# Kernel optimization log

Measured on AMD Instinct MI355X. Metric: run time of the kernel, lower is better.

## Reference

```python
import jax, jax.numpy as jnp
import numpy as np

N = 50000      # nodes
E = 60000      # edges
F_IN = 32      # num_features
DIM = 64       # hidden dim
B = 256        # graphs in batch


def setup_inputs() -> dict:
    key = jax.random.key(0)
    ks = jax.random.split(key, 18)
    s = 0.05
    rn = lambda k, shp: (jax.random.normal(k, shp, jnp.float32) * s)
    return {
        "x": jax.random.normal(ks[0], (N, F_IN), jnp.float32),
        "edge_index": jax.random.randint(ks[1], (2, E), 0, N),
        "batch": jnp.sort(jax.random.randint(ks[2], (N,), 0, B)),
        "lin0_w": rn(ks[3], (DIM, F_IN)), "lin0_b": rn(ks[4], (DIM,)),
        "nn1_w": rn(ks[5], (DIM, 1)), "nn1_b": rn(ks[6], (DIM,)),
        "nn2_w": rn(ks[7], (DIM * DIM, DIM)), "nn2_b": rn(ks[8], (DIM * DIM,)),
        "conv_b": rn(ks[9], (DIM,)),
        "gru_w_ih": rn(ks[10], (3 * DIM, DIM)), "gru_w_hh": rn(ks[11], (3 * DIM, DIM)),
        "gru_b_ih": rn(ks[12], (3 * DIM,)), "gru_b_hh": rn(ks[13], (3 * DIM,)),
        "lstm_w_ih": rn(ks[14], (4 * DIM, 2 * DIM)), "lstm_w_hh": rn(ks[15], (4 * DIM, DIM)),
        "lstm_b_ih": rn(ks[16], (4 * DIM,)), "lstm_b_hh": rn(ks[17], (4 * DIM,)),
    }


def reference(x, edge_index, batch, lin0_w, lin0_b, nn1_w, nn1_b, nn2_w, nn2_b,
              conv_b, gru_w_ih, gru_w_hh, gru_b_ih, gru_b_hh,
              lstm_w_ih, lstm_w_hh, lstm_b_ih, lstm_b_hh):
    src, dst = edge_index[0], edge_index[1]
    n_nodes = x.shape[0]
    out = jax.nn.relu(x @ lin0_w.T + lin0_b)          # [N, DIM]
    h = out                                            # GRU hidden state
    edge_attr = jnp.ones((edge_index.shape[1], 1), x.dtype)  # as in source forward
    ones_e = jnp.ones((edge_index.shape[1],), x.dtype)
    deg = jax.ops.segment_sum(ones_e, dst, num_segments=n_nodes)
    inv_deg = jnp.where(deg > 0, 1.0 / jnp.maximum(deg, 1.0), 0.0)[:, None]

    for _ in range(3):
        # edge-conditioned weight: MLP(edge_attr) -> [E, DIM, DIM]
        ew = (jax.nn.relu(edge_attr @ nn1_w.T + nn1_b) @ nn2_w.T + nn2_b)
        ew = ew.reshape(-1, DIM, DIM)
        msg = jnp.einsum('ei,eio->eo', out[src], ew)   # per-edge matvec
        agg = jax.ops.segment_sum(msg, dst, num_segments=n_nodes) * inv_deg  # scatter-mean
        m = jax.nn.relu(agg + conv_b)
        # GRU cell (seq_len = 1)
        gi = m @ gru_w_ih.T + gru_b_ih
        gh = h @ gru_w_hh.T + gru_b_hh
        i_r, i_z, i_n = jnp.split(gi, 3, axis=-1)
        h_r, h_z, h_n = jnp.split(gh, 3, axis=-1)
        r = jax.nn.sigmoid(i_r + h_r)
        z = jax.nn.sigmoid(i_z + h_z)
        n = jnp.tanh(i_n + r * h_n)
        h = (1.0 - z) * n + z * h
        out = h
    feat_map = out

    # Set2Set pooling, 3 processing steps, LSTM(2*DIM -> DIM)
    q_star = jnp.zeros((B, 2 * DIM), x.dtype)
    hl = jnp.zeros((B, DIM), x.dtype)
    cl = jnp.zeros((B, DIM), x.dtype)
    for _ in range(3):
        gates = q_star @ lstm_w_ih.T + lstm_b_ih + hl @ lstm_w_hh.T + lstm_b_hh
        ig, fg, gg, og = jnp.split(gates, 4, axis=-1)  # torch gate order i,f,g,o
        cl = jax.nn.sigmoid(fg) * cl + jax.nn.sigmoid(ig) * jnp.tanh(gg)
        hl = jax.nn.sigmoid(og) * jnp.tanh(cl)
        e = jnp.sum(out * hl[batch], axis=-1)          # [N]
        emax = jax.ops.segment_max(e, batch, num_segments=B)
        emax = jnp.where(jnp.isfinite(emax), emax, 0.0)
        a = jnp.exp(e - emax[batch])
        asum = jax.ops.segment_sum(a, batch, num_segments=B)
        a = a / (asum[batch] + 1e-16)                  # segment softmax
        r_vec = jax.ops.segment_sum(a[:, None] * out, batch, num_segments=B)
        q_star = jnp.concatenate([hl, r_vec], axis=-1)
    return q_star, feat_map
```

## Files before the change

### kernel.cpp

```cpp
#include <hip/hip_runtime.h>
#include <math.h>

#define NN 50000
#define NE 60000
#define FIN 32
#define DIM 64
#define NGB 256
#define SCB 196

typedef short s8v __attribute__((ext_vector_type(8)));
typedef float f4v __attribute__((ext_vector_type(4)));

__device__ __forceinline__ float rl(float v, int lane) {
    return __int_as_float(__builtin_amdgcn_readlane(__float_as_int(v), lane));
}
__device__ __forceinline__ float sigm(float x) { return 1.f / (1.f + expf(-x)); }

__device__ __forceinline__ unsigned int pk2(float a, float b) {
    unsigned int ua = __float_as_uint(a);
    unsigned int ub = __float_as_uint(b);
    ua = (ua + 0x7FFFu + ((ua >> 16) & 1u)) >> 16;
    ub = (ub + 0x7FFFu + ((ub >> 16) & 1u)) & 0xFFFF0000u;
    return ua | ub;
}
__device__ __forceinline__ unsigned short pk1(float a) {
    unsigned int ua = __float_as_uint(a);
    return (unsigned short)((ua + 0x7FFFu + ((ua >> 16) & 1u)) >> 16);
}
__device__ __forceinline__ s8v as_s8(uint4 u) {
    union { uint4 a; s8v b; } c; c.a = u; return c.b;
}

__global__ void k_precompute_W(const float* __restrict__ nn1_w, const float* __restrict__ nn1_b,
                               const float* __restrict__ nn2_w, const float* __restrict__ nn2_b,
                               float* __restrict__ W) {
    __shared__ float t[64];
    int tid = threadIdx.x;
    if (tid < 64) t[tid] = fmaxf(nn1_w[tid] + nn1_b[tid], 0.f);
    __syncthreads();
    int k = blockIdx.x * blockDim.x + tid;
    float acc = nn2_b[k];
    #pragma unroll
    for (int j = 0; j < 64; ++j) acc += t[j] * nn2_w[k * 64 + j];
    W[k] = acc;
}

__global__ void k_pack_mfma(const float* __restrict__ W, const float* __restrict__ wih,
                            const float* __restrict__ whh, const float* __restrict__ bih,
                            const float* __restrict__ bhh, unsigned int* __restrict__ P,
                            float* __restrict__ brz) {
    int q = blockIdx.x * 256 + threadIdx.x;
    if (q < 128) brz[q] = bih[q] + bhh[q];
    if (q < 2048) {
        int byte = q * 4, col = byte >> 7, rem = byte & 127;
        int lin = rem ^ ((col & 7) << 4);
        int k0 = (lin >> 4) * 8 + ((lin >> 2) & 3) * 2;
        P[q] = pk2(W[k0 * 64 + col], W[(k0 + 1) * 64 + col]);
    } else if (q < 10240) {
        int w = q - 2048, byte = w * 4, col = byte >> 8, rem = byte & 255;
        int lin = rem ^ ((col & 7) << 4);
        int k0 = (lin >> 4) * 8 + ((lin >> 2) & 3) * 2;
        int g = col >> 6, o = col & 63;
        int rowbase = (g * 64 + o) * 64;
        const float* src = (k0 >= 64) ? whh : wih;
        int kk = (k0 >= 64) ? k0 - 64 : k0;
        P[q] = pk2(src[rowbase + kk], src[rowbase + kk + 1]);
    } else if (q < 12288) {
        int w = q - 10240, byte = w * 4, col = byte >> 7, rem = byte & 127;
        int lin = rem ^ ((col & 7) << 4);
        int k0 = (lin >> 4) * 8 + ((lin >> 2) & 3) * 2;
        P[q] = pk2(wih[(128 + col) * 64 + k0], wih[(128 + col) * 64 + k0 + 1]);
    } else {
        int w = q - 12288, byte = w * 4, col = byte >> 7, rem = byte & 127;
        int lin = rem ^ ((col & 7) << 4);
        int k0 = (lin >> 4) * 8 + ((lin >> 2) & 3) * 2;
        P[q] = pk2(whh[(128 + col) * 64 + k0], whh[(128 + col) * 64 + k0 + 1]);
    }
}

__global__ void k_transpose_lstm(const float* __restrict__ wih, const float* __restrict__ whh,
                                 float* __restrict__ wihT, float* __restrict__ whhT) {
    int p = blockIdx.x * 256 + threadIdx.x;
    if (p < 256 * 128) { int o = p >> 7, k = p & 127; wihT[k * 256 + o] = wih[p]; }
    if (p < 256 * 64)  { int o = p >> 6, k = p & 63;  whhT[k * 256 + o] = whh[p]; }
}

__global__ void k_degi(const int* __restrict__ ei, int* __restrict__ degc) {
    int i = blockIdx.x * 256 + threadIdx.x;
    if (i < NE) atomicAdd(&degc[ei[NE + i]], 1);
}

__global__ void k_bsum(const int* __restrict__ degc, int* __restrict__ bsum) {
    __shared__ int red[256];
    int t = threadIdx.x;
    int idx = blockIdx.x * 256 + t;
    red[t] = (idx < NN) ? degc[idx] : 0;
    __syncthreads();
    for (int off = 128; off; off >>= 1) {
        if (t < off) red[t] += red[t + off];
        __syncthreads();
    }
    if (t == 0) bsum[blockIdx.x] = red[0];
}

__global__ void k_emit(const int* __restrict__ degc, const int* __restrict__ bsum,
                       int* __restrict__ rowptr, int* __restrict__ cur) {
    __shared__ int bo[256];
    __shared__ int sc[256];
    int t = threadIdx.x;
    int idx = blockIdx.x * 256 + t;
    bo[t] = (t < blockIdx.x) ? bsum[t] : 0;
    __syncthreads();
    for (int off = 128; off; off >>= 1) {
        if (t < off) bo[t] += bo[t + off];
        __syncthreads();
    }
    int boff = bo[0];
    int v = (idx < NN) ? degc[idx] : 0;
    sc[t] = v;
    __syncthreads();
    for (int off = 1; off < 256; off <<= 1) {
        int u = (t >= off) ? sc[t - off] : 0;
        __syncthreads();
        sc[t] += u;
        __syncthreads();
    }
    if (idx <= NN) {
        int excl = boff + sc[t] - v;
        rowptr[idx] = excl;
        if (idx < NN) cur[idx] = excl;
    }
}

__global__ void k_fill(const int* __restrict__ ei, int* __restrict__ cur,
                       int* __restrict__ adj) {
    int i = blockIdx.x * 256 + threadIdx.x;
    if (i < NE) {
        int s = ei[i], d = ei[NE + i];
        int pos = atomicAdd(&cur[d], 1);
        adj[pos] = s;
    }
}

__global__ void k_bounds(const int* __restrict__ batch, int* __restrict__ starts,
                         int* __restrict__ cnt) {
    __shared__ int sLB[257];
    int b = threadIdx.x;
    int lo = 0, hi = NN;
    while (lo < hi) {
        int mid = (lo + hi) >> 1;
        if (batch[mid] < b) lo = mid + 1; else hi = mid;
    }
    sLB[b] = lo;
    if (b == 0) sLB[256] = NN;
    __syncthreads();
    starts[b] = sLB[b];
    cnt[b] = sLB[b + 1] - sLB[b];
}

__global__ void k_lin0(const float* __restrict__ x, const float* __restrict__ w,
                       const float* __restrict__ b, float* __restrict__ h) {
    __shared__ float wT[FIN * 64];
    int tid = threadIdx.x;
    for (int p = tid; p < FIN * 64; p += 256) {
        int k = p >> 6, o = p & 63;
        wT[p] = w[o * FIN + k];
    }
    __syncthreads();
    int l = tid & 63;
    float bl = b[l];
    int wave = blockIdx.x * 4 + (tid >> 6);
    int nwaves = gridDim.x * 4;
    for (int n0 = wave * 2; n0 < NN; n0 += nwaves * 2) {
        float xv0 = x[n0 * FIN + (l & 31)];
        float xv1 = x[(n0 + 1) * FIN + (l & 31)];
        float a0 = bl, a1 = bl;
        #pragma unroll
        for (int k = 0; k < FIN; ++k) {
            float wk = wT[k * 64 + l];
            a0 += rl(xv0, k) * wk;
            a1 += rl(xv1, k) * wk;
        }
        h[n0 * 64 + l] = fmaxf(a0, 0.f);
        h[(n0 + 1) * 64 + l] = fmaxf(a1, 0.f);
    }
}

__global__ void __launch_bounds__(256) k_update(
    const float* __restrict__ hin, const int* __restrict__ rowptr,
    const int* __restrict__ adj, const unsigned int* __restrict__ P,
    const float* __restrict__ conv_b, const float* __restrict__ brz,
    const float* __restrict__ bih, const float* __restrict__ bhh,
    float* __restrict__ hout) {
    __shared__ unsigned int L[16384];
    int tid = threadIdx.x;
    #pragma unroll
    for (int p = 0; p < 14336; p += 256) L[p + tid] = P[p + tid];
    __syncthreads();

    int l = tid & 63;
    int w = tid >> 6;
    int nb = (blockIdx.x * 4 + w) * 16;
    if (nb >= NN) return;
    int row = l & 15, kq = l >> 4;
    int node = nb + row;

    int es = rowptr[node], ee = rowptr[node + 1];
    float g0x = 0.f, g0y = 0.f, g0z = 0.f, g0w = 0.f;
    float g1x = 0.f, g1y = 0.f, g1z = 0.f, g1w = 0.f;
    float g2x = 0.f, g2y = 0.f, g2z = 0.f, g2w = 0.f;
    float g3x = 0.f, g3y = 0.f, g3z = 0.f, g3w = 0.f;
    for (int k = es; k < ee; ++k) {
        int src = adj[k];
        const float4* hp0 = (const float4*)(hin + src * 64 + kq * 8);
        const float4* hp1 = (const float4*)(hin + src * 64 + 32 + kq * 8);
        float4 v0 = hp0[0], v1 = hp0[1], v2 = hp1[0], v3 = hp1[1];
        g0x += v0.x; g0y += v0.y; g0z += v0.z; g0w += v0.w;
        g1x += v1.x; g1y += v1.y; g1z += v1.z; g1w += v1.w;
        g2x += v2.x; g2y += v2.y; g2z += v2.z; g2w += v2.w;
        g3x += v3.x; g3y += v3.y; g3z += v3.z; g3w += v3.w;
    }
    float dv = (float)(ee - es);
    float inv = dv > 0.f ? 1.f / dv : 0.f;

    uint4 aA[2];
    aA[0].x = pk2(g0x * inv, g0y * inv);
    aA[0].y = pk2(g0z * inv, g0w * inv);
    aA[0].z = pk2(g1x * inv, g1y * inv);
    aA[0].w = pk2(g1z * inv, g1w * inv);
    aA[1].x = pk2(g2x * inv, g2y * inv);
    aA[1].y = pk2(g2z * inv, g2w * inv);
    aA[1].z = pk2(g3x * inv, g3y * inv);
    aA[1].w = pk2(g3z * inv, g3w * inv);

    f4v mC[4];
    #pragma unroll
    for (int ct = 0; ct < 4; ++ct) {
        f4v acc = {0.f, 0.f, 0.f, 0.f};
        int col = ct * 16 + row;
        #pragma unroll
        for (int kt = 0; kt < 2; ++kt) {
            int boff = col * 128 + ((kt * 64 + kq * 16) ^ ((col & 7) << 4));
            uint4 b = *(const uint4*)((const char*)L + boff);
            acc = __builtin_amdgcn_mfma_f32_16x16x32_bf16(as_s8(aA[kt]), as_s8(b), acc, 0, 0, 0);
        }
        mC[ct] = acc;
    }

    int mbase = 57344 + w * 2048;
    #pragma unroll
    for (int ct = 0; ct < 4; ++ct) {
        int ch = ct * 16 + row;
        float cb = conv_b[ch];
        #pragma unroll
        for (int r = 0; r < 4; ++r) {
            float mval = fmaxf(mC[ct][r] + cb, 0.f);
            int nrow = kq * 4 + r;
            int off = mbase + ((nrow * 128 + ch * 2) ^ ((nrow & 7) << 4));
            *(unsigned short*)((char*)L + off) = pk1(mval);
        }
    }
    uint4 mA[2], hA[2];
    #pragma unroll
    for (int kt = 0; kt < 2; ++kt) {
        int off = mbase + ((row * 128 + kt * 64 + kq * 16) ^ ((row & 7) << 4));
        mA[kt] = *(const uint4*)((const char*)L + off);
        const float4* hs = (const float4*)(hin + node * 64 + kt * 32 + kq * 8);
        float4 y0 = hs[0], y1 = hs[1];
        hA[kt].x = pk2(y0.x, y0.y);
        hA[kt].y = pk2(y0.z, y0.w);
        hA[kt].z = pk2(y1.x, y1.y);
        hA[kt].w = pk2(y1.z, y1.w);
    }

    f4v g01[8];
    #pragma unroll
    for (int ct = 0; ct < 8; ++ct) {
        f4v acc = {0.f, 0.f, 0.f, 0.f};
        int col = ct * 16 + row;
        #pragma unroll
        for (int kt = 0; kt < 4; ++kt) {
            uint4 a = (kt < 2) ? mA[kt] : hA[kt - 2];
            int boff = 8192 + col * 256 + ((kt * 64 + kq * 16) ^ ((col & 7) << 4));
            uint4 b = *(const uint4*)((const char*)L + boff);
            acc = __builtin_amdgcn_mfma_f32_16x16x32_bf16(as_s8(a), as_s8(b), acc, 0, 0, 0);
        }
        g01[ct] = acc;
    }
    f4v gin[4], ghn[4];
    #pragma unroll
    for (int ct = 0; ct < 4; ++ct) {
        f4v ai = {0.f, 0.f, 0.f, 0.f}, ah = {0.f, 0.f, 0.f, 0.f};
        int col = ct * 16 + row;
        #pragma unroll
        for (int kt = 0; kt < 2; ++kt) {
            int swz = (kt * 64 + kq * 16) ^ ((col & 7) << 4);
            uint4 bi = *(const uint4*)((const char*)L + 40960 + col * 128 + swz);
            uint4 bh = *(const uint4*)((const char*)L + 49152 + col * 128 + swz);
            ai = __builtin_amdgcn_mfma_f32_16x16x32_bf16(as_s8(mA[kt]), as_s8(bi), ai, 0, 0, 0);
            ah = __builtin_amdgcn_mfma_f32_16x16x32_bf16(as_s8(hA[kt]), as_s8(bh), ah, 0, 0, 0);
        }
        gin[ct] = ai; ghn[ct] = ah;
    }

    #pragma unroll
    for (int ct = 0; ct < 4; ++ct) {
        int ch = ct * 16 + row;
        float br = brz[ch], bz = brz[64 + ch];
        float bin = bih[128 + ch], bhn = bhh[128 + ch];
        #pragma unroll
        for (int r = 0; r < 4; ++r) {
            int n2 = nb + kq * 4 + r;
            float rg = sigm(g01[ct][r] + br);
            float zg = sigm(g01[4 + ct][r] + bz);
            float ng = tanhf(gin[ct][r] + bin + rg * (ghn[ct][r] + bhn));
            float hold = hin[n2 * 64 + ch];
            hout[n2 * 64 + ch] = (1.f - zg) * ng + zg * hold;
        }
    }
}

__global__ void __launch_bounds__(1024) k_s2s(
    const float* __restrict__ h, const int* __restrict__ starts,
    const int* __restrict__ cnt, const float* __restrict__ wihT,
    const float* __restrict__ whhT, const float* __restrict__ bih,
    const float* __restrict__ bhh, float* __restrict__ hl,
    float* __restrict__ cl, float* __restrict__ qstar, int first) {
    __shared__ float ga[256];
    __shared__ float hlv[64];
    __shared__ float mw[16], ssw[16];
    __shared__ float accw[16][64];
    int b = blockIdx.x, tid = threadIdx.x, w = tid >> 6, l = tid & 63;

    if (first) {
        if (tid < 64) {
            float ig = sigm(bih[tid] + bhh[tid]);
            float gg = tanhf(bih[128 + tid] + bhh[128 + tid]);
            float og = sigm(bih[192 + tid] + bhh[192 + tid]);
            float c = ig * gg;
            cl[b * 64 + tid] = c;
            float hh = og * tanhf(c);
            hl[b * 64 + tid] = hh;
            hlv[tid] = hh;
        }
    } else {
        if (tid < 256) {
            const float* qs = qstar + b * 128;
            const float* hb = hl + b * 64;
            float a = bih[tid] + bhh[tid];
            for (int k = 0; k < 128; ++k) a += qs[k] * wihT[k * 256 + tid];
            for (int k = 0; k < 64; ++k)  a += hb[k] * whhT[k * 256 + tid];
            ga[tid] = a;
        }
        __syncthreads();
        if (tid < 64) {
            float c = sigm(ga[64 + tid]) * cl[b * 64 + tid] + sigm(ga[tid]) * tanhf(ga[128 + tid]);
            cl[b * 64 + tid] = c;
            float hh = sigm(ga[192 + tid]) * tanhf(c);
            hl[b * 64 + tid] = hh;
            hlv[tid] = hh;
        }
    }
    __syncthreads();

    int s = starts[b], c = cnt[b];
    float hld = hlv[l];
    float m = -1e30f, ss = 0.f, racc = 0.f;
    for (int i = w; i < c; i += 16) {
        float hv = h[(s + i) * 64 + l];
        float v = hv * hld;
        #pragma unroll
        for (int off = 32; off; off >>= 1) v += __shfl_xor(v, off, 64);
        float nm = fmaxf(m, v);
        float scale = expf(m - nm);
        float p = expf(v - nm);
        ss = ss * scale + p;
        racc = racc * scale + p * hv;
        m = nm;
    }
    if (l == 0) { mw[w] = m; ssw[w] = ss; }
    accw[w][l] = racc;
    __syncthreads();
    if (tid < 64) {
        float M = -1e30f;
        #pragma unroll
        for (int q = 0; q < 16; ++q) M = fmaxf(M, mw[q]);
        float asum = 0.f, r = 0.f;
        #pragma unroll
        for (int q = 0; q < 16; ++q) {
            float f = expf(mw[q] - M);
            asum += ssw[q] * f;
            r += accw[q][tid] * f;
        }
        qstar[b * 128 + tid] = hlv[tid];
        qstar[b * 128 + 64 + tid] = r / (asum + 1e-16f);
    }
}

extern "C" void kernel_launch(void* const* d_in, const int* in_sizes, int n_in,
                              void* d_out, int out_size, void* d_ws, size_t ws_size,
                              hipStream_t stream) {
    const float* x      = (const float*)d_in[0];
    const int*   ei     = (const int*)  d_in[1];
    const int*   batch  = (const int*)  d_in[2];
    const float* lin0_w = (const float*)d_in[3];
    const float* lin0_b = (const float*)d_in[4];
    const float* nn1_w  = (const float*)d_in[5];
    const float* nn1_b  = (const float*)d_in[6];
    const float* nn2_w  = (const float*)d_in[7];
    const float* nn2_b  = (const float*)d_in[8];
    const float* conv_b = (const float*)d_in[9];
    const float* gwih   = (const float*)d_in[10];
    const float* gwhh   = (const float*)d_in[11];
    const float* gbih   = (const float*)d_in[12];
    const float* gbhh   = (const float*)d_in[13];
    const float* lwih   = (const float*)d_in[14];
    const float* lwhh   = (const float*)d_in[15];
    const float* lbih   = (const float*)d_in[16];
    const float* lbhh   = (const float*)d_in[17];

    float* qstar = (float*)d_out;
    float* hdo   = (float*)d_out + NGB * 128;

    float* ws     = (float*)d_ws;
    float* W      = ws;
    float* hbuf   = ws + 4096;
    int*   rowptr = (int*)(hbuf + NN * 64);
    int*   curp   = rowptr + NN + 1;
    int*   adj    = curp + NN;
    int*   degc   = adj + NE;
    int*   bsum   = degc + NN;
    int*   cnt    = bsum + 256;
    int*   starts = cnt + 256;
    float* hl     = (float*)(starts + 256);
    float* cl     = hl + NGB * 64;
    float* wihT   = cl + NGB * 64;
    float* whhT   = wihT + 128 * 256;
    unsigned int* P = (unsigned int*)(whhT + 64 * 256);
    float* brz    = (float*)(P + 14336);

    hipMemsetAsync(degc, 0, NN * sizeof(int), stream);

    k_precompute_W<<<16, 256, 0, stream>>>(nn1_w, nn1_b, nn2_w, nn2_b, W);
    k_pack_mfma<<<56, 256, 0, stream>>>(W, gwih, gwhh, gbih, gbhh, P, brz);
    k_transpose_lstm<<<128, 256, 0, stream>>>(lwih, lwhh, wihT, whhT);
    k_degi<<<(NE + 255) / 256, 256, 0, stream>>>(ei, degc);
    k_bsum<<<SCB, 256, 0, stream>>>(degc, bsum);
    k_emit<<<SCB, 256, 0, stream>>>(degc, bsum, rowptr, curp);
    k_fill<<<(NE + 255) / 256, 256, 0, stream>>>(ei, curp, adj);
    k_bounds<<<1, 256, 0, stream>>>(batch, starts, cnt);
    k_lin0<<<512, 256, 0, stream>>>(x, lin0_w, lin0_b, hbuf);

    k_update<<<782, 256, 0, stream>>>(hbuf, rowptr, adj, P, conv_b, brz, gbih, gbhh, hdo);
    k_update<<<782, 256, 0, stream>>>(hdo, rowptr, adj, P, conv_b, brz, gbih, gbhh, hbuf);
    k_update<<<782, 256, 0, stream>>>(hbuf, rowptr, adj, P, conv_b, brz, gbih, gbhh, hdo);

    for (int st = 0; st < 3; ++st) {
        k_s2s<<<NGB, 1024, 0, stream>>>(hdo, starts, cnt, wihT, whhT, lbih, lbhh,
                                        hl, cl, qstar, st == 0 ? 1 : 0);
    }
}
```

Measured before the change: 250.6 us.

## Fuse setup kernels and merge three Set2Set steps into one launch

Folds the edge-weight MLP precompute into the MFMA packing kernel and does the degree-buffer zeroing there, which removes the memset and a launch. The LSTM transpose and batch-bounds search are merged into the degree-count kernel. The three Set2Set launches become one kernel that keeps the LSTM state in shared memory across steps. This cuts the launch count from about 15 to 9 and drops global round trips for hl/cl, at the cost of some redundant MLP dot products in the packing kernel.

New measurement: 297.0 us. +18.5%, slower.

```diff
diff --git a/kernel.cpp b/kernel.cpp
--- a/kernel.cpp
+++ b/kernel.cpp
@@ -31,31 +31,34 @@
     union { uint4 a; s8v b; } c; c.a = u; return c.b;
 }
 
-__global__ void k_precompute_W(const float* __restrict__ nn1_w, const float* __restrict__ nn1_b,
-                               const float* __restrict__ nn2_w, const float* __restrict__ nn2_b,
-                               float* __restrict__ W) {
+__global__ void k_pack_mfma(const float* __restrict__ nn1_w, const float* __restrict__ nn1_b,
+                            const float* __restrict__ nn2_w, const float* __restrict__ nn2_b,
+                            const float* __restrict__ wih, const float* __restrict__ whh,
+                            const float* __restrict__ bih, const float* __restrict__ bhh,
+                            unsigned int* __restrict__ P, float* __restrict__ brz,
+                            int* __restrict__ degc) {
     __shared__ float t[64];
     int tid = threadIdx.x;
     if (tid < 64) t[tid] = fmaxf(nn1_w[tid] + nn1_b[tid], 0.f);
     __syncthreads();
-    int k = blockIdx.x * blockDim.x + tid;
-    float acc = nn2_b[k];
-    #pragma unroll
-    for (int j = 0; j < 64; ++j) acc += t[j] * nn2_w[k * 64 + j];
-    W[k] = acc;
-}
-
-__global__ void k_pack_mfma(const float* __restrict__ W, const float* __restrict__ wih,
-                            const float* __restrict__ whh, const float* __restrict__ bih,
-                            const float* __restrict__ bhh, unsigned int* __restrict__ P,
-                            float* __restrict__ brz) {
-    int q = blockIdx.x * 256 + threadIdx.x;
+    int q = blockIdx.x * 256 + tid;
+    #pragma unroll
+    for (int z = 0; z < 4; ++z) {
+        int idx = q * 4 + z;
+        if (idx < NN) degc[idx] = 0;
+    }
     if (q < 128) brz[q] = bih[q] + bhh[q];
     if (q < 2048) {
         int byte = q * 4, col = byte >> 7, rem = byte & 127;
         int lin = rem ^ ((col & 7) << 4);
         int k0 = (lin >> 4) * 8 + ((lin >> 2) & 3) * 2;
-        P[q] = pk2(W[k0 * 64 + col], W[(k0 + 1) * 64 + col]);
+        int ka = k0 * 64 + col, kb = (k0 + 1) * 64 + col;
+        float w0 = nn2_b[ka], w1 = nn2_b[kb];
+        #pragma unroll
+        for (int j = 0; j < 64; ++j) w0 += t[j] * nn2_w[ka * 64 + j];
+        #pragma unroll
+        for (int j = 0; j < 64; ++j) w1 += t[j] * nn2_w[kb * 64 + j];
+        P[q] = pk2(w0, w1);
     } else if (q < 10240) {
         int w = q - 2048, byte = w * 4, col = byte >> 8, rem = byte & 255;
         int lin = rem ^ ((col & 7) << 4);
@@ -78,16 +81,30 @@
     }
 }
 
-__global__ void k_transpose_lstm(const float* __restrict__ wih, const float* __restrict__ whh,
-                                 float* __restrict__ wihT, float* __restrict__ whhT) {
-    int p = blockIdx.x * 256 + threadIdx.x;
-    if (p < 256 * 128) { int o = p >> 7, k = p & 127; wihT[k * 256 + o] = wih[p]; }
-    if (p < 256 * 64)  { int o = p >> 6, k = p & 63;  whhT[k * 256 + o] = whh[p]; }
-}
-
-__global__ void k_degi(const int* __restrict__ ei, int* __restrict__ degc) {
-    int i = blockIdx.x * 256 + threadIdx.x;
+__global__ void k_prep(const int* __restrict__ ei, int* __restrict__ degc,
+                       const float* __restrict__ lwih, const float* __restrict__ lwhh,
+                       float* __restrict__ wihT, float* __restrict__ whhT,
+                       const int* __restrict__ batch, int* __restrict__ starts,
+                       int* __restrict__ cnt) {
+    int tid = threadIdx.x;
+    int i = blockIdx.x * 256 + tid;
     if (i < NE) atomicAdd(&degc[ei[NE + i]], 1);
+    if (i < 256 * 128) { int o = i >> 7, k = i & 127; wihT[k * 256 + o] = lwih[i]; }
+    if (i < 256 * 64)  { int o = i >> 6, k = i & 63;  whhT[k * 256 + o] = lwhh[i]; }
+    if (blockIdx.x == 234) {
+        __shared__ int sLB[257];
+        int b = tid;
+        int lo = 0, hi = NN;
+        while (lo < hi) {
+            int mid = (lo + hi) >> 1;
+            if (batch[mid] < b) lo = mid + 1; else hi = mid;
+        }
+        sLB[b] = lo;
+        if (b == 0) sLB[256] = NN;
+        __syncthreads();
+        starts[b] = sLB[b];
+        cnt[b] = sLB[b + 1] - sLB[b];
+    }
 }
 
 __global__ void k_bsum(const int* __restrict__ degc, int* __restrict__ bsum) {
@@ -140,22 +157,6 @@
         int pos = atomicAdd(&cur[d], 1);
         adj[pos] = s;
     }
-}
-
-__global__ void k_bounds(const int* __restrict__ batch, int* __restrict__ starts,
-                         int* __restrict__ cnt) {
-    __shared__ int sLB[257];
-    int b = threadIdx.x;
-    int lo = 0, hi = NN;
-    while (lo < hi) {
-        int mid = (lo + hi) >> 1;
-        if (batch[mid] < b) lo = mid + 1; else hi = mid;
-    }
-    sLB[b] = lo;
-    if (b == 0) sLB[256] = NN;
-    __syncthreads();
-    starts[b] = sLB[b];
-    cnt[b] = sLB[b + 1] - sLB[b];
 }
 
 __global__ void k_lin0(const float* __restrict__ x, const float* __restrict__ w,
@@ -320,80 +321,81 @@
     }
 }
 
-__global__ void __launch_bounds__(1024) k_s2s(
+__global__ void __launch_bounds__(1024) k_s2s_all(
     const float* __restrict__ h, const int* __restrict__ starts,
     const int* __restrict__ cnt, const float* __restrict__ wihT,
     const float* __restrict__ whhT, const float* __restrict__ bih,
-    const float* __restrict__ bhh, float* __restrict__ hl,
-    float* __restrict__ cl, float* __restrict__ qstar, int first) {
+    const float* __restrict__ bhh, float* __restrict__ qstar) {
     __shared__ float ga[256];
-    __shared__ float hlv[64];
+    __shared__ float qs[128];
+    __shared__ float hlv[64], clv[64];
     __shared__ float mw[16], ssw[16];
     __shared__ float accw[16][64];
     int b = blockIdx.x, tid = threadIdx.x, w = tid >> 6, l = tid & 63;
-
-    if (first) {
+    int s = starts[b], c = cnt[b];
+
+    for (int st = 0; st < 3; ++st) {
+        if (st == 0) {
+            if (tid < 64) {
+                float ig = sigm(bih[tid] + bhh[tid]);
+                float gg = tanhf(bih[128 + tid] + bhh[128 + tid]);
+                float og = sigm(bih[192 + tid] + bhh[192 + tid]);
+                float cc = ig * gg;
+                clv[tid] = cc;
+                hlv[tid] = og * tanhf(cc);
+            }
+        } else {
+            if (tid < 256) {
+                float a = bih[tid] + bhh[tid];
+                for (int k = 0; k < 128; ++k) a += qs[k] * wihT[k * 256 + tid];
+                for (int k = 0; k < 64; ++k)  a += hlv[k] * whhT[k * 256 + tid];
+                ga[tid] = a;
+            }
+            __syncthreads();
+            if (tid < 64) {
+                float cc = sigm(ga[64 + tid]) * clv[tid] + sigm(ga[tid]) * tanhf(ga[128 + tid]);
+                clv[tid] = cc;
+                hlv[tid] = sigm(ga[192 + tid]) * tanhf(cc);
+            }
+        }
+        __syncthreads();
+
+        float hld = hlv[l];
+        float m = -1e30f, ss = 0.f, racc = 0.f;
+        for (int i = w; i < c; i += 16) {
+            float hv = h[(s + i) * 64 + l];
+            float v = hv * hld;
+            #pragma unroll
+            for (int off = 32; off; off >>= 1) v += __shfl_xor(v, off, 64);
+            float nm = fmaxf(m, v);
+            float scale = expf(m - nm);
+            float p = expf(v - nm);
+            ss = ss * scale + p;
+            racc = racc * scale + p * hv;
+            m = nm;
+        }
+        if (l == 0) { mw[w] = m; ssw[w] = ss; }
+        accw[w][l] = racc;
+        __syncthreads();
         if (tid < 64) {
-            float ig = sigm(bih[tid] + bhh[tid]);
-            float gg = tanhf(bih[128 + tid] + bhh[128 + tid]);
-            float og = sigm(bih[192 + tid] + bhh[192 + tid]);
-            float c = ig * gg;
-            cl[b * 64 + tid] = c;
-            float hh = og * tanhf(c);
-            hl[b * 64 + tid] = hh;
-            hlv[tid] = hh;
-        }
-    } else {
-        if (tid < 256) {
-            const float* qs = qstar + b * 128;
-            const float* hb = hl + b * 64;
-            float a = bih[tid] + bhh[tid];
-            for (int k = 0; k < 128; ++k) a += qs[k] * wihT[k * 256 + tid];
-            for (int k = 0; k < 64; ++k)  a += hb[k] * whhT[k * 256 + tid];
-            ga[tid] = a;
-        }
-        __syncthreads();
-        if (tid < 64) {
-            float c = sigm(ga[64 + tid]) * cl[b * 64 + tid] + sigm(ga[tid]) * tanhf(ga[128 + tid]);
-            cl[b * 64 + tid] = c;
-            float hh = sigm(ga[192 + tid]) * tanhf(c);
-            hl[b * 64 + tid] = hh;
-            hlv[tid] = hh;
-        }
-    }
-    __syncthreads();
-
-    int s = starts[b], c = cnt[b];
-    float hld = hlv[l];
-    float m = -1e30f, ss = 0.f, racc = 0.f;
-    for (int i = w; i < c; i += 16) {
-        float hv = h[(s + i) * 64 + l];
-        float v = hv * hld;
-        #pragma unroll
-        for (int off = 32; off; off >>= 1) v += __shfl_xor(v, off, 64);
-        float nm = fmaxf(m, v);
-        float scale = expf(m - nm);
-        float p = expf(v - nm);
-        ss = ss * scale + p;
-        racc = racc * scale + p * hv;
-        m = nm;
-    }
-    if (l == 0) { mw[w] = m; ssw[w] = ss; }
-    accw[w][l] = racc;
-    __syncthreads();
+            float M = -1e30f;
+            #pragma unroll
+            for (int q = 0; q < 16; ++q) M = fmaxf(M, mw[q]);
+            float asum = 0.f, r = 0.f;
+            #pragma unroll
+            for (int q = 0; q < 16; ++q) {
+                float f = expf(mw[q] - M);
+                asum += ssw[q] * f;
+                r += accw[q][tid] * f;
+            }
+            qs[tid] = hlv[tid];
+            qs[64 + tid] = r / (asum + 1e-16f);
+        }
+        __syncthreads();
+    }
     if (tid < 64) {
-        float M = -1e30f;
-        #pragma unroll
-        for (int q = 0; q < 16; ++q) M = fmaxf(M, mw[q]);
-        float asum = 0.f, r = 0.f;
-        #pragma unroll
-        for (int q = 0; q < 16; ++q) {
-            float f = expf(mw[q] - M);
-            asum += ssw[q] * f;
-            r += accw[q][tid] * f;
-        }
-        qstar[b * 128 + tid] = hlv[tid];
-        qstar[b * 128 + 64 + tid] = r / (asum + 1e-16f);
+        qstar[b * 128 + tid] = qs[tid];
+        qstar[b * 128 + 64 + tid] = qs[64 + tid];
     }
 }
 
@@ -423,8 +425,7 @@
     float* hdo   = (float*)d_out + NGB * 128;
 
     float* ws     = (float*)d_ws;
-    float* W      = ws;
-    float* hbuf   = ws + 4096;
+    float* hbuf   = ws;
     int*   rowptr = (int*)(hbuf + NN * 64);
     int*   curp   = rowptr + NN + 1;
     int*   adj    = curp + NN;
@@ -432,31 +433,23 @@
     int*   bsum   = degc + NN;
     int*   cnt    = bsum + 256;
     int*   starts = cnt + 256;
-    float* hl     = (float*)(starts + 256);
-    float* cl     = hl + NGB * 64;
-    float* wihT   = cl + NGB * 64;
+    float* wihT   = (float*)(starts + 256);
     float* whhT   = wihT + 128 * 256;
     unsigned int* P = (unsigned int*)(whhT + 64 * 256);
     float* brz    = (float*)(P + 14336);
 
-    hipMemsetAsync(degc, 0, NN * sizeof(int), stream);
-
-    k_precompute_W<<<16, 256, 0, stream>>>(nn1_w, nn1_b, nn2_w, nn2_b, W);
-    k_pack_mfma<<<56, 256, 0, stream>>>(W, gwih, gwhh, gbih, gbhh, P, brz);
-    k_transpose_lstm<<<128, 256, 0, stream>>>(lwih, lwhh, wihT, whhT);
-    k_degi<<<(NE + 255) / 256, 256, 0, stream>>>(ei, degc);
+    k_pack_mfma<<<56, 256, 0, stream>>>(nn1_w, nn1_b, nn2_w, nn2_b, gwih, gwhh,
+                                        gbih, gbhh, P, brz, degc);
+    k_prep<<<(NE + 255) / 256, 256, 0, stream>>>(ei, degc, lwih, lwhh, wihT, whhT,
+                                                 batch, starts, cnt);
     k_bsum<<<SCB, 256, 0, stream>>>(degc, bsum);
     k_emit<<<SCB, 256, 0, stream>>>(degc, bsum, rowptr, curp);
     k_fill<<<(NE + 255) / 256, 256, 0, stream>>>(ei, curp, adj);
-    k_bounds<<<1, 256, 0, stream>>>(batch, starts, cnt);
     k_lin0<<<512, 256, 0, stream>>>(x, lin0_w, lin0_b, hbuf);
 
     k_update<<<782, 256, 0, stream>>>(hbuf, rowptr, adj, P, conv_b, brz, gbih, gbhh, hdo);
     k_update<<<782, 256, 0, stream>>>(hdo, rowptr, adj, P, conv_b, brz, gbih, gbhh, hbuf);
     k_update<<<782, 256, 0, stream>>>(hbuf, rowptr, adj, P, conv_b, brz, gbih, gbhh, hdo);
 
-    for (int st = 0; st < 3; ++st) {
-        k_s2s<<<NGB, 1024, 0, stream>>>(hdo, starts, cnt, wihT, whhT, lbih, lbhh,
-                                        hl, cl, qstar, st == 0 ? 1 : 0);
-    }
-}
+    k_s2s_all<<<NGB, 1024, 0, stream>>>(hdo, starts, cnt, wihT, whhT, lbih, lbhh, qstar);
+}
```
